# Kernel optimization log

Measured on AMD Instinct MI355X. Metric: run time of the kernel, lower is better.

Reference implementation:

```python
import jax, jax.numpy as jnp
import numpy as np

EPS = 1e-6

def _l2norm_axis1(x):
    # torch Normalize(2): divide by L2 norm over dim 1 (the T axis of [B,T,F])
    return x / jnp.sqrt(jnp.sum(x * x, axis=1, keepdims=True))

def _mlp(x, w1, b1, w2, b2):
    # frame_MLPEmbed / freq_MLPEmbed share structure: linear-relu-linear-l2norm(dim=1)
    h = jax.nn.relu(x @ w1 + b1)
    return _l2norm_axis1(h @ w2 + b2)

def _reshape_feat(f):
    # [L,B,C,T,D] -> permute(0,2,1,3) per layer -> [L,B,T,C*D]
    L, B, C, T, D = f.shape
    return jnp.transpose(f, (0, 1, 3, 2, 4)).reshape(L, B, T, C * D)

def _cos_time(x):
    # x: [L,B,T,C]; cosine sims between frames within each batch item -> [L,B,T,T]
    xn = x / (jnp.sqrt(jnp.sum(x * x, axis=-1, keepdims=True)) + EPS)
    S = (jnp.einsum('lbtc,lbsc->lbts', xn, xn) + 1.0) * 0.5
    return S / jnp.sum(S, axis=-1, keepdims=True)

def _cos_freq(x):
    # cosine sims between batch items per frame, returned as [L,B,T,B]
    xn = x / (jnp.sqrt(jnp.sum(x * x, axis=-1, keepdims=True)) + EPS)
    S = (jnp.einsum('lbtc,latc->lbta', xn, xn) + 1.0) * 0.5
    return S / jnp.sum(S, axis=-1, keepdims=True)

def _forward(feat_s, feat_t, tk_w1, tk_b1, tk_w2, tk_b2, fk_w1, fk_b1, fk_w2, fk_b2,
             tq_w1, tq_b1, tq_w2, tq_b2, fq_w1, fq_b1, fq_w2, fq_b2):
    feat_t = jax.lax.stop_gradient(feat_t)  # detach=True
    xs = _reshape_feat(feat_s)  # [s_len,B,T,CD]
    xt = _reshape_feat(feat_t)  # [t_len,B,T,CD]
    s_len, t_len = xs.shape[0], xt.shape[0]

    # gram matrices used for key/query MLPs
    sim_t = jnp.einsum('lbtc,lbsc->lbts', xt, xt)    # [t_len,B,T,T]
    sim_t_g = jnp.einsum('lbtc,latc->lbta', xt, xt)  # [t_len,B,T,B]
    sim_s = jnp.einsum('lbtc,lbsc->lbts', xs, xs)    # [s_len,B,T,T]
    sim_s_g = jnp.einsum('lbtc,latc->lbta', xs, xs)  # [s_len,B,T,B]

    mlp_v = jax.vmap(_mlp)  # vmap over the per-layer MLPs
    tk = mlp_v(sim_t, tk_w1, tk_b1, tk_w2, tk_b2)     # [t_len,B,T,T]
    fk = mlp_v(sim_t_g, fk_w1, fk_b1, fk_w2, fk_b2)   # [t_len,B,T,32]
    tq = mlp_v(sim_s, tq_w1, tq_b1, tq_w2, tq_b2)     # [s_len,B,T,T]
    fq = mlp_v(sim_s_g, fq_w1, fq_b1, fq_w2, fq_b2)   # [s_len,B,T,32]

    time_key = jnp.moveaxis(tk, 0, -1)    # [B,T,T,t_len]
    freq_key = jnp.moveaxis(fk, 0, -1)    # [B,T,32,t_len]
    time_query = jnp.moveaxis(tq, 0, 2)   # [B,T,s_len,T]
    freq_query = jnp.moveaxis(fq, 0, 2)   # [B,T,s_len,32]

    time_att = jax.nn.softmax(jnp.matmul(time_query, time_key), axis=-1)  # [B,T,s_len,t_len]
    freq_att = jax.nn.softmax(jnp.matmul(freq_query, freq_key), axis=-1)  # [B,T,s_len,t_len]

    stu_time = _cos_time(xs)  # [s_len,B,T,T]
    tea_time = _cos_time(xt)  # [t_len,B,T,T]
    stu_freq = _cos_freq(xs)  # [s_len,B,T,B]
    tea_freq = _cos_freq(xt)  # [t_len,B,T,B]

    # the torch nested lists are [i][j]; student entries depend only on i, teacher only on j
    stu_time_b = jnp.broadcast_to(stu_time[:, None], (s_len, t_len) + stu_time.shape[1:])
    stu_freq_b = jnp.broadcast_to(stu_freq[:, None], (s_len, t_len) + stu_freq.shape[1:])
    tea_time_b = jnp.broadcast_to(tea_time[None, :], (s_len, t_len) + tea_time.shape[1:])
    tea_freq_b = jnp.broadcast_to(tea_freq[None, :], (s_len, t_len) + tea_freq.shape[1:])

    return (stu_time_b, stu_freq_b, tea_time_b, tea_freq_b, time_att, freq_att)

def setup_inputs() -> dict:
    key = jax.random.key(0)
    ks = jax.random.split(key, 20)
    s_len, t_len, B, C, T, D = 4, 4, 8, 64, 256, 16
    H = 2 * T  # frame MLP hidden
    F = 32     # bsz * factor
    p = lambda k, shp: jax.random.normal(k, shp, dtype=jnp.float32) * 0.02
    return {
        'feat_s': jax.random.normal(ks[0], (s_len, B, C, T, D), dtype=jnp.float32),
        'feat_t': jax.random.normal(ks[1], (t_len, B, C, T, D), dtype=jnp.float32),
        'tk_w1': p(ks[2], (t_len, T, H)), 'tk_b1': p(ks[3], (t_len, H)),
        'tk_w2': p(ks[4], (t_len, H, T)), 'tk_b2': p(ks[5], (t_len, T)),
        'fk_w1': p(ks[6], (t_len, B, F)), 'fk_b1': p(ks[7], (t_len, F)),
        'fk_w2': p(ks[8], (t_len, F, F)), 'fk_b2': p(ks[9], (t_len, F)),
        'tq_w1': p(ks[10], (s_len, T, H)), 'tq_b1': p(ks[11], (s_len, H)),
        'tq_w2': p(ks[12], (s_len, H, T)), 'tq_b2': p(ks[13], (s_len, T)),
        'fq_w1': p(ks[14], (s_len, B, F)), 'fq_b1': p(ks[15], (s_len, F)),
        'fq_w2': p(ks[16], (s_len, F, F)), 'fq_b2': p(ks[17], (s_len, F)),
    }

def reference(feat_s, feat_t, tk_w1, tk_b1, tk_w2, tk_b2, fk_w1, fk_b1, fk_w2, fk_b2,
              tq_w1, tq_b1, tq_w2, tq_b2, fq_w1, fq_b1, fq_w2, fq_b2):
    return _forward(feat_s, feat_t, tk_w1, tk_b1, tk_w2, tk_b2, fk_w1, fk_b1, fk_w2, fk_b2,
                    tq_w1, tq_b1, tq_w2, tq_b2, fq_w1, fq_b1, fq_w2, fq_b2)
```

## Files before the change

### kernel.cpp

```cpp
#include <hip/hip_runtime.h>
#include <math.h>

typedef _Float16 half_t;
typedef _Float16 h2 __attribute__((ext_vector_type(2)));
typedef _Float16 h4 __attribute__((ext_vector_type(4)));
typedef _Float16 h8 __attribute__((ext_vector_type(8)));
typedef float f4 __attribute__((ext_vector_type(4)));
static constexpr float REPS = 1e-6f;

__global__ __launch_bounds__(256) void k_prep2(const float* __restrict__ tkw1, const float* __restrict__ tqw1,
                                               const float* __restrict__ tkw2, const float* __restrict__ tqw2,
                                               const float* __restrict__ tkb1, const float* __restrict__ tqb1,
                                               const float* __restrict__ tkb2, const float* __restrict__ tqb2,
                                               half_t* __restrict__ W1t, half_t* __restrict__ W2t,
                                               float* __restrict__ Bc1, float* __restrict__ Bc2,
                                               float* __restrict__ part,
                                               const float* __restrict__ fs, const float* __restrict__ ft,
                                               half_t* __restrict__ Xh, float* __restrict__ nrm) {
  __shared__ float T[64][65];
  int bid = blockIdx.x;
  int tid = threadIdx.x;
  if (bid < 256) {
    int z = bid >> 5, tile = bid & 31;
    int kt = tile >> 3, ntile = tile & 7;
    const float* src = (z < 4 ? tkw1 : tqw1) + (size_t)(z & 3) * 256 * 512;
#pragma unroll
    for (int q = 0; q < 16; q++) {
      int e = q * 256 + tid;
      int r = e >> 6, c = e & 63;
      T[r][c] = src[(size_t)(kt * 64 + r) * 512 + ntile * 64 + c];
    }
    __syncthreads();
#pragma unroll
    for (int q = 0; q < 16; q++) {
      int e = q * 256 + tid;
      int nn = e >> 6, kk = e & 63;
      W1t[(size_t)z * 512 * 256 + (size_t)(ntile * 64 + nn) * 256 + kt * 64 + kk] = (half_t)T[kk][nn];
    }
  } else if (bid < 512) {
    int bb = bid - 256;
    int z = bb >> 5, tile = bb & 31;
    int kt = tile >> 2, ntile = tile & 3;
    const float* src = (z < 4 ? tkw2 : tqw2) + (size_t)(z & 3) * 512 * 256;
#pragma unroll
    for (int q = 0; q < 16; q++) {
      int e = q * 256 + tid;
      int r = e >> 6, c = e & 63;
      T[r][c] = src[(size_t)(kt * 64 + r) * 256 + ntile * 64 + c];
    }
    __syncthreads();
#pragma unroll
    for (int q = 0; q < 16; q++) {
      int e = q * 256 + tid;
      int nn = e >> 6, kk = e & 63;
      W2t[(size_t)z * 256 * 512 + (size_t)(ntile * 64 + nn) * 512 + kt * 64 + kk] = (half_t)T[kk][nn];
    }
  } else if (bid == 512) {
    for (int e = tid; e < 4096; e += 256) {
      int z = e >> 9, n = e & 511;
      Bc1[e] = (z < 4 ? tkb1 : tqb1)[(z & 3) * 512 + n];
    }
    for (int e = tid; e < 2048; e += 256) {
      int z = e >> 8, n = e & 255;
      Bc2[e] = (z < 4 ? tkb2 : tqb2)[(z & 3) * 256 + n];
    }
    for (int e = tid; e < 16384; e += 256) part[e] = 0.f;
  } else {
    int bid2 = bid - 513;
    int tensor = bid2 >> 7;
    int l = (bid2 >> 5) & 3;
    int b = (bid2 >> 2) & 7;
    int tc = bid2 & 3;
    int tl = tid >> 2;
    int d0 = (tid & 3) * 4;
    int t = tc * 64 + tl;
    const float* base = (tensor ? ft : fs) + (size_t)((l * 8 + b) * 64) * 4096 + t * 16 + d0;
    size_t row = (size_t)(tensor * 32 + l * 8 + b) * 256 + t;
    half_t* xrow = Xh + row * 1024 + d0;
    float acc = 0.f;
#pragma unroll 8
    for (int c = 0; c < 64; c++) {
      float4 v = *(const float4*)(base + (size_t)c * 4096);
      acc += v.x * v.x + v.y * v.y + v.z * v.z + v.w * v.w;
      h4 hv;
      hv[0] = (half_t)v.x; hv[1] = (half_t)v.y; hv[2] = (half_t)v.z; hv[3] = (half_t)v.w;
      *(h4*)(xrow + c * 16) = hv;
    }
    acc += __shfl_xor(acc, 1);
    acc += __shfl_xor(acc, 2);
    if ((tid & 3) == 0) nrm[row] = sqrtf(acc);
  }
}

__global__ __launch_bounds__(512) void k_gs(const half_t* __restrict__ Xh,
                                            const float* __restrict__ nrm,
                                            half_t* __restrict__ simh,
                                            float* __restrict__ out_stu,
                                            float* __restrict__ out_tea,
                                            float* __restrict__ simg) {
  __shared__ __align__(16) char smem[35584];
  int bid = blockIdx.x;
  int tid = threadIdx.x;
  if (bid < 256) {
    half_t* Bsm = (half_t*)smem;
    float* Tile = (float*)smem;
    float* rspart = (float*)(smem + 33280);
    float* rowsumS = (float*)(smem + 34304);
    float* invn = (float*)(smem + 34560);
    int mt = bid & 3;
    int z = bid >> 2;
    const half_t* Bb = Xh + (size_t)z * 256 * 1024;
    int w = tid >> 6, lane = tid & 63;
    int wm = w >> 2, wn = w & 3;
    int lr = lane & 15, lg = lane >> 4;
    f4 acc[2][4] = {};
    int r0 = tid >> 3, seg0 = tid & 7;
    int sw0 = (seg0 ^ (r0 & 7)) * 8;
    h8 bv[4], bv2[4];
#pragma unroll
    for (int it = 0; it < 4; it++)
      bv[it] = *(const h8*)(Bb + (size_t)(it * 64 + r0) * 1024 + seg0 * 8);
    for (int kc = 0; kc < 1024; kc += 64) {
      __syncthreads();
#pragma unroll
      for (int it = 0; it < 4; it++)
        *(h8*)(Bsm + (it * 64 + r0) * 64 + sw0) = bv[it];
      __syncthreads();
      if (kc + 64 < 1024) {
#pragma unroll
        for (int it = 0; it < 4; it++)
          bv2[it] = *(const h8*)(Bb + (size_t)(it * 64 + r0) * 1024 + kc + 64 + seg0 * 8);
      }
#pragma unroll
      for (int kk = 0; kk < 2; kk++) {
        int g = kk * 4 + lg;
        h8 af[2], bf[4];
#pragma unroll
        for (int mf = 0; mf < 2; mf++) {
          int rA = mt * 64 + wm * 32 + mf * 16 + lr;
          af[mf] = *(const h8*)(Bsm + rA * 64 + ((g ^ (rA & 7)) * 8));
        }
#pragma unroll
        for (int nf = 0; nf < 4; nf++) {
          int rB = wn * 64 + nf * 16 + lr;
          bf[nf] = *(const h8*)(Bsm + rB * 64 + ((g ^ (rB & 7)) * 8));
        }
#pragma unroll
        for (int mf = 0; mf < 2; mf++)
#pragma unroll
          for (int nf = 0; nf < 4; nf++)
            acc[mf][nf] = __builtin_amdgcn_mfma_f32_16x16x32_f16(af[mf], bf[nf], acc[mf][nf], 0, 0, 0);
      }
      if (kc + 64 < 1024) {
#pragma unroll
        for (int it = 0; it < 4; it++) bv[it] = bv2[it];
      }
    }
    int tensor = z >> 5, l = (z >> 3) & 3, b = z & 7;
    const float* nz = nrm + z * 256;
    if (tid < 256) invn[tid] = 1.f / (nz[tid] + REPS);
    __syncthreads();
    int cols[4];
#pragma unroll
    for (int nf = 0; nf < 4; nf++) cols[nf] = wn * 64 + nf * 16 + lr;
    float rowpart[2][4];
#pragma unroll
    for (int mf = 0; mf < 2; mf++)
#pragma unroll
      for (int rg = 0; rg < 4; rg++) {
        int rib = wm * 32 + mf * 16 + lg * 4 + rg;
        float invr = invn[mt * 64 + rib];
        float p = 0.f;
#pragma unroll
        for (int nf = 0; nf < 4; nf++)
          p += fmaf(acc[mf][nf][rg] * (invr * invn[cols[nf]]), 0.5f, 0.5f);
        rowpart[mf][rg] = p;
      }
#pragma unroll
    for (int mf = 0; mf < 2; mf++)
#pragma unroll
      for (int rg = 0; rg < 4; rg++) {
        float p = rowpart[mf][rg];
        p += __shfl_xor(p, 1); p += __shfl_xor(p, 2);
        p += __shfl_xor(p, 4); p += __shfl_xor(p, 8);
        rowpart[mf][rg] = p;
      }
    if (lr == 0) {
#pragma unroll
      for (int mf = 0; mf < 2; mf++)
#pragma unroll
        for (int rg = 0; rg < 4; rg++)
          rspart[(wm * 32 + mf * 16 + lg * 4 + rg) * 4 + wn] = rowpart[mf][rg];
    }
    __syncthreads();
    if (tid < 64)
      rowsumS[tid] = 1.f / (rspart[tid * 4] + rspart[tid * 4 + 1] +
                            rspart[tid * 4 + 2] + rspart[tid * 4 + 3]);
    __syncthreads();
    float* outp = tensor ? out_tea : out_stu;
    for (int ph = 0; ph < 2; ph++) {
      if (wm == ph) {
#pragma unroll
        for (int mf = 0; mf < 2; mf++)
#pragma unroll
          for (int nf = 0; nf < 4; nf++)
#pragma unroll
            for (int rg = 0; rg < 4; rg++)
              Tile[(mf * 16 + lg * 4 + rg) * 260 + cols[nf]] = acc[mf][nf][rg];
      }
      __syncthreads();
#pragma unroll
      for (int it2 = 0; it2 < 4; it2++) {
        int fid = it2 * 512 + tid;
        int row = fid >> 6;
        int col = (fid & 63) << 2;
        int rib = ph * 32 + row;
        int t = mt * 64 + rib;
        float4 S4 = *(const float4*)(Tile + row * 260 + col);
        float invnr = invn[t];
        float rinv = rowsumS[rib];
        float4 vv;
        vv.x = fmaf(S4.x * (invnr * invn[col + 0]), 0.5f, 0.5f) * rinv;
        vv.y = fmaf(S4.y * (invnr * invn[col + 1]), 0.5f, 0.5f) * rinv;
        vv.z = fmaf(S4.z * (invnr * invn[col + 2]), 0.5f, 0.5f) * rinv;
        vv.w = fmaf(S4.w * (invnr * invn[col + 3]), 0.5f, 0.5f) * rinv;
        h4 sh;
        sh[0] = (half_t)S4.x; sh[1] = (half_t)S4.y;
        sh[2] = (half_t)S4.z; sh[3] = (half_t)S4.w;
        *(h4*)(simh + (size_t)z * 65536 + (size_t)t * 256 + col) = sh;
        size_t inner = ((size_t)(b * 256 + t)) * 256 + col;
        if (tensor == 0) {
          size_t base = (size_t)l * 4 * 524288;
#pragma unroll
          for (int j = 0; j < 4; j++)
            *(float4*)(outp + base + (size_t)j * 524288 + inner) = vv;
        } else {
#pragma unroll
          for (int i2 = 0; i2 < 4; i2++)
            *(float4*)(outp + ((size_t)(i2 * 4 + l)) * 524288 + inner) = vv;
        }
      }
      __syncthreads();
    }
  } else {
    half_t* X = (half_t*)smem;
    float* red = (float*)(smem + 33280);
    int sb = bid - 256;
    int tensor = sb >> 8;
    int l = (sb >> 6) & 3;
    int tc = sb & 63;
    int t0 = tc * 4;
    int kg = tid >> 8;
    int inner = tid & 255;
    int tl_c = inner >> 6;
    int ab = inner & 63;
    int bb = ab >> 3, aa = ab & 7;
    float acc = 0.f;
    for (int kh = 0; kh < 2; kh++) {
#pragma unroll
      for (int j = 0; j < 4; j++) {
        int i = j * 512 + tid;
        int r = i >> 6, col = i & 63;
        int b = r & 7, tl = r >> 3;
        const half_t* src = Xh + ((size_t)(tensor * 32 + l * 8 + b) * 256 + t0 + tl) * 1024
                               + kh * 512 + col * 8;
        *(h8*)(X + r * 520 + col * 8) = *(const h8*)src;
      }
      __syncthreads();
      {
        const half_t* xa = X + (tl_c * 8 + bb) * 520 + kg * 256;
        const half_t* xb = X + (tl_c * 8 + aa) * 520 + kg * 256;
#pragma unroll 8
        for (int k = 0; k < 256; k += 8) {
          h8 va = *(const h8*)(xa + k);
          h8 vb = *(const h8*)(xb + k);
#if __has_builtin(__builtin_amdgcn_fdot2)
#pragma unroll
          for (int i = 0; i < 4; i++) {
            h2 pa, pb;
            pa[0] = va[2 * i]; pa[1] = va[2 * i + 1];
            pb[0] = vb[2 * i]; pb[1] = vb[2 * i + 1];
            acc = __builtin_amdgcn_fdot2(pa, pb, acc, false);
          }
#else
#pragma unroll
          for (int e = 0; e < 8; e++) acc += (float)va[e] * (float)vb[e];
#endif
        }
      }
      __syncthreads();
    }
    if (kg == 1) red[inner] = acc;
    __syncthreads();
    if (kg == 0)
      simg[(size_t)tensor * 65536 + ((size_t)(l * 8 + bb) * 256 + t0 + tl_c) * 8 + aa] =
          acc + red[inner];
  }
}

__global__ __launch_bounds__(256) void k_m1s(const half_t* __restrict__ simh,
                                             const half_t* __restrict__ W1t,
                                             const float* __restrict__ Bc1,
                                             half_t* __restrict__ hbuf,
                                             const float* __restrict__ simg,
                                             const float* __restrict__ n,
                                             float* __restrict__ out_stu, float* __restrict__ out_tea,
                                             const float* __restrict__ qw1, const float* __restrict__ qb1,
                                             const float* __restrict__ qw2, const float* __restrict__ qb2,
                                             const float* __restrict__ kw1, const float* __restrict__ kb1,
                                             const float* __restrict__ kw2, const float* __restrict__ kb2,
                                             float* __restrict__ qout, float* __restrict__ kout) {
  __shared__ __align__(16) char smem[40352];
  int bid = blockIdx.x;
  int tid = threadIdx.x;
  if (bid < 512) {
    constexpr int K = 256, N = 512;
    half_t* Asm = (half_t*)smem;
    half_t* Bsm = (half_t*)(smem + 16384);
    int mt = bid & 15, nt = (bid >> 4) & 3, z = bid >> 6;
    int l = z & 3, path = z >> 2;
    const half_t* Ab = simh + ((size_t)((path == 0 ? 32 : 0) + l * 8)) * 256 * 256;
    const half_t* Bb = W1t + (size_t)z * 512 * 256;
    half_t* Ob = hbuf + (size_t)z * 2048 * 512;
    int wave = tid >> 6, lane = tid & 63;
    int wm = (wave >> 1) * 64, wn = (wave & 1) * 64;
    int lr = lane & 15, lg = lane >> 4;
    f4 acc[4][4] = {};
    int r0 = tid >> 3, seg0 = tid & 7;
    int sw0 = (seg0 ^ (r0 & 7)) * 8;
    h8 av[4], bv[4], av2[4], bv2[4];
#pragma unroll
    for (int j = 0; j < 4; j++) {
      av[j] = *(const h8*)(Ab + (size_t)(mt * 128 + r0 + 32 * j) * K + seg0 * 8);
      bv[j] = *(const h8*)(Bb + (size_t)(nt * 128 + r0 + 32 * j) * K + seg0 * 8);
    }
    for (int kc = 0; kc < K; kc += 64) {
      __syncthreads();
#pragma unroll
      for (int j = 0; j < 4; j++) {
        *(h8*)(Asm + (r0 + 32 * j) * 64 + sw0) = av[j];
        *(h8*)(Bsm + (r0 + 32 * j) * 64 + sw0) = bv[j];
      }
      __syncthreads();
      if (kc + 64 < K) {
#pragma unroll
        for (int j = 0; j < 4; j++) {
          av2[j] = *(const h8*)(Ab + (size_t)(mt * 128 + r0 + 32 * j) * K + kc + 64 + seg0 * 8);
          bv2[j] = *(const h8*)(Bb + (size_t)(nt * 128 + r0 + 32 * j) * K + kc + 64 + seg0 * 8);
        }
      }
#pragma unroll
      for (int kk = 0; kk < 2; kk++) {
        h8 af[4], bf[4];
#pragma unroll
        for (int mf = 0; mf < 4; mf++) {
          int r = wm + mf * 16 + lr;
          af[mf] = *(const h8*)(Asm + r * 64 + (((kk * 4 + lg) ^ (r & 7)) * 8));
        }
#pragma unroll
        for (int nf = 0; nf < 4; nf++) {
          int r = wn + nf * 16 + lr;
          bf[nf] = *(const h8*)(Bsm + r * 64 + (((kk * 4 + lg) ^ (r & 7)) * 8));
        }
#pragma unroll
        for (int mf = 0; mf < 4; mf++)
#pragma unroll
          for (int nf = 0; nf < 4; nf++)
            acc[mf][nf] = __builtin_amdgcn_mfma_f32_16x16x32_f16(af[mf], bf[nf], acc[mf][nf], 0, 0, 0);
      }
      if (kc + 64 < K) {
#pragma unroll
        for (int j = 0; j < 4; j++) { av[j] = av2[j]; bv[j] = bv2[j]; }
      }
    }
#pragma unroll
    for (int nf = 0; nf < 4; nf++) {
      int col = nt * 128 + wn + nf * 16 + lr;
      float bv3 = Bc1[z * N + col];
#pragma unroll
      for (int mf = 0; mf < 4; mf++) {
#pragma unroll
        for (int rg = 0; rg < 4; rg++) {
          int row = mt * 128 + wm + mf * 16 + lg * 4 + rg;
          float v = fmaxf(acc[mf][nf][rg] + bv3, 0.f);
          Ob[(size_t)row * N + col] = (half_t)v;
        }
      }
    }
  } else if (bid < 576) {
    int bb = bid - 512;
    int tensor = bb >> 5;
    int lb = bb & 31;
    const float* sg = simg + (size_t)tensor * 65536;
    const float* nb2 = n + tensor * 8192;
    float* out = tensor ? out_tea : out_stu;
    int l = lb >> 3, b = lb & 7;
    int a = tid & 7;
    for (int tc = 0; tc < 8; tc++) {
      int t = tc * 32 + (tid >> 3);
      float nb = nb2[lb * 256 + t] + REPS;
      float na = nb2[(l * 8 + a) * 256 + t] + REPS;
      float v = (sg[((size_t)lb * 256 + t) * 8 + a] / (nb * na) + 1.f) * 0.5f;
      float w = v;
      for (int m = 1; m < 8; m <<= 1) w += __shfl_xor(w, m);
      v /= w;
      size_t inner = ((size_t)(b * 256 + t)) * 8 + a;
      if (tensor == 0) {
#pragma unroll
        for (int j = 0; j < 4; j++) out[((size_t)(l * 4 + j)) * 16384 + inner] = v;
      } else {
#pragma unroll
        for (int i = 0; i < 4; i++) out[((size_t)(i * 4 + l)) * 16384 + inner] = v;
      }
    }
  } else {
    float* sw1 = (float*)smem;
    float* sb1 = (float*)(smem + 1024);
    float* sw2 = (float*)(smem + 1152);
    float* sb2 = (float*)(smem + 5248);
    float* zs  = (float*)(smem + 5376);
    float* pcn = (float*)(smem + 39168);
    float* cn  = (float*)(smem + 40224);
    int bb = bid - 576;
    int tensor = bb >> 5;
    int lb = bb & 31;
    int l = lb >> 3;
    const float* w1 = tensor ? kw1 : qw1;
    const float* b1 = tensor ? kb1 : qb1;
    const float* w2 = tensor ? kw2 : qw2;
    const float* b2 = tensor ? kb2 : qb2;
    const float* sg = simg + (size_t)tensor * 65536;
    float* outp = tensor ? kout : qout;
    int t = tid;
    sw1[t] = w1[l * 256 + t];
    if (t < 32) { sb1[t] = b1[l * 32 + t]; sb2[t] = b2[l * 32 + t]; }
    for (int q = t; q < 1024; q += 256) sw2[q] = w2[l * 1024 + q];
    __syncthreads();
    float x[8];
#pragma unroll
    for (int a = 0; a < 8; a++) x[a] = sg[((size_t)lb * 256 + t) * 8 + a];
    float h[32];
#pragma unroll
    for (int f = 0; f < 32; f++) {
      float acc = sb1[f];
#pragma unroll
      for (int a = 0; a < 8; a++) acc += x[a] * sw1[a * 32 + f];
      h[f] = fmaxf(acc, 0.f);
    }
#pragma unroll
    for (int g = 0; g < 32; g++) {
      float acc = sb2[g];
#pragma unroll
      for (int f = 0; f < 32; f++) acc += h[f] * sw2[f * 32 + g];
      zs[t * 33 + g] = acc;
    }
    __syncthreads();
    {
      int col = t & 31, ch = t >> 5;
      float sq = 0.f;
      for (int r = ch * 32; r < ch * 32 + 32; r++) { float v = zs[r * 33 + col]; sq += v * v; }
      pcn[ch * 33 + col] = sq;
    }
    __syncthreads();
    if (t < 32) {
      float ssum = 0.f;
#pragma unroll
      for (int c = 0; c < 8; c++) ssum += pcn[c * 33 + t];
      cn[t] = sqrtf(ssum);
    }
    __syncthreads();
#pragma unroll
    for (int g = 0; g < 32; g++)
      outp[((size_t)lb * 256 + t) * 32 + g] = zs[t * 33 + g] / cn[g];
  }
}

__global__ __launch_bounds__(256) void k_mfma2(const half_t* __restrict__ A,
                                               const half_t* __restrict__ Bt,
                                               const float* __restrict__ bias,
                                               half_t* __restrict__ out,
                                               float* __restrict__ part) {
  constexpr int K = 512, N = 256;
  __shared__ __align__(16) half_t Asm[128 * 64];
  __shared__ __align__(16) half_t Bsm[128 * 64];
  int z = blockIdx.z;
  const half_t* Ab = A + (size_t)z * 2048 * 512;
  const half_t* Bb = Bt + (size_t)z * 256 * 512;
  half_t* Ob = out + (size_t)z * 2048 * 256;
  int mt = blockIdx.x, nt = blockIdx.y;
  int tid = threadIdx.x;
  int wave = tid >> 6, lane = tid & 63;
  int wm = (wave >> 1) * 64, wn = (wave & 1) * 64;
  int lr = lane & 15, lg = lane >> 4;
  f4 acc[4][4] = {};
  int r0 = tid >> 3, seg0 = tid & 7;
  int sw0 = (seg0 ^ (r0 & 7)) * 8;
  h8 av[4], bv[4], av2[4], bv2[4];
#pragma unroll
  for (int j = 0; j < 4; j++) {
    av[j] = *(const h8*)(Ab + (size_t)(mt * 128 + r0 + 32 * j) * K + seg0 * 8);
    bv[j] = *(const h8*)(Bb + (size_t)(nt * 128 + r0 + 32 * j) * K + seg0 * 8);
  }
  for (int kc = 0; kc < K; kc += 64) {
    __syncthreads();
#pragma unroll
    for (int j = 0; j < 4; j++) {
      *(h8*)(Asm + (r0 + 32 * j) * 64 + sw0) = av[j];
      *(h8*)(Bsm + (r0 + 32 * j) * 64 + sw0) = bv[j];
    }
    __syncthreads();
    if (kc + 64 < K) {
#pragma unroll
      for (int j = 0; j < 4; j++) {
        av2[j] = *(const h8*)(Ab + (size_t)(mt * 128 + r0 + 32 * j) * K + kc + 64 + seg0 * 8);
        bv2[j] = *(const h8*)(Bb + (size_t)(nt * 128 + r0 + 32 * j) * K + kc + 64 + seg0 * 8);
      }
    }
#pragma unroll
    for (int kk = 0; kk < 2; kk++) {
      h8 af[4], bf[4];
#pragma unroll
      for (int mf = 0; mf < 4; mf++) {
        int r = wm + mf * 16 + lr;
        af[mf] = *(const h8*)(Asm + r * 64 + (((kk * 4 + lg) ^ (r & 7)) * 8));
      }
#pragma unroll
      for (int nf = 0; nf < 4; nf++) {
        int r = wn + nf * 16 + lr;
        bf[nf] = *(const h8*)(Bsm + r * 64 + (((kk * 4 + lg) ^ (r & 7)) * 8));
      }
#pragma unroll
      for (int mf = 0; mf < 4; mf++)
#pragma unroll
        for (int nf = 0; nf < 4; nf++)
          acc[mf][nf] = __builtin_amdgcn_mfma_f32_16x16x32_f16(af[mf], bf[nf], acc[mf][nf], 0, 0, 0);
    }
    if (kc + 64 < K) {
#pragma unroll
      for (int j = 0; j < 4; j++) { av[j] = av2[j]; bv[j] = bv2[j]; }
    }
  }
#pragma unroll
  for (int nf = 0; nf < 4; nf++) {
    int col = nt * 128 + wn + nf * 16 + lr;
    float bv3 = bias[z * N + col];
    float colsq = 0.f;
#pragma unroll
    for (int mf = 0; mf < 4; mf++) {
#pragma unroll
      for (int rg = 0; rg < 4; rg++) {
        int row = mt * 128 + wm + mf * 16 + lg * 4 + rg;
        float v = acc[mf][nf][rg] + bv3;
        Ob[(size_t)row * N + col] = (half_t)v;
        colsq += v * v;
      }
    }
    colsq += __shfl_xor(colsq, 16);
    colsq += __shfl_xor(colsq, 32);
    if (lg == 0) {
      int b = mt >> 1;
      atomicAdd(&part[((z * 8 + b) << 8) + col], colsq);
    }
  }
}

__global__ __launch_bounds__(256) void k_att(const half_t* __restrict__ Zq,
                                             const half_t* __restrict__ Zk,
                                             const float* __restrict__ part,
                                             const float* __restrict__ fq,
                                             const float* __restrict__ fk,
                                             float* __restrict__ out_time,
                                             float* __restrict__ out_freq) {
  __shared__ float invq[4][256], invk[4][256];
  int bid = blockIdx.x;
  int tid = threadIdx.x;
  if (bid < 128) {
    int b = bid >> 4, tc = bid & 15;
    for (int e = tid; e < 1024; e += 256) {
      int i = e >> 8, s = e & 255;
      invq[i][s] = rsqrtf(part[(((4 + i) * 8 + b) << 8) + s]);
      invk[i][s] = rsqrtf(part[((i * 8 + b) << 8) + s]);
    }
    __syncthreads();
    int w = tid >> 6, lane = tid & 63;
    int s0 = lane * 4;
#pragma unroll
    for (int tt = 0; tt < 4; tt++) {
      int t = tc * 16 + w * 4 + tt;
      float qv[4][4], kv[4][4];
#pragma unroll
      for (int i = 0; i < 4; i++) {
        size_t lbO = (size_t)(i * 8 + b);
        h4 qh = *(const h4*)(Zq + (lbO * 256 + t) * 256 + s0);
        h4 kh = *(const h4*)(Zk + (lbO * 256 + t) * 256 + s0);
#pragma unroll
        for (int e = 0; e < 4; e++) {
          qv[i][e] = (float)qh[e] * invq[i][s0 + e];
          kv[i][e] = (float)kh[e] * invk[i][s0 + e];
        }
      }
      float acc[4][4];
#pragma unroll
      for (int i = 0; i < 4; i++)
#pragma unroll
        for (int j = 0; j < 4; j++) {
          float a = 0.f;
#pragma unroll
          for (int e = 0; e < 4; e++) a += qv[i][e] * kv[j][e];
          acc[i][j] = a;
        }
#pragma unroll
      for (int i = 0; i < 4; i++)
#pragma unroll
        for (int j = 0; j < 4; j++)
          for (int m = 32; m >= 1; m >>= 1) acc[i][j] += __shfl_xor(acc[i][j], m);
      if (lane < 16) {
        int i = lane >> 2, j = lane & 3;
        float mx = fmaxf(fmaxf(acc[i][0], acc[i][1]), fmaxf(acc[i][2], acc[i][3]));
        float sum = expf(acc[i][0] - mx) + expf(acc[i][1] - mx) + expf(acc[i][2] - mx) + expf(acc[i][3] - mx);
        out_time[((size_t)(b * 256 + t)) * 16 + lane] = expf(acc[i][j] - mx) / sum;
      }
    }
  } else {
    int sub = tid >> 6, lane = tid & 63;
    int pair = (bid - 128) * 4 + sub;
    int b = pair >> 7, tp = pair & 127;
    int t = tp * 2 + (lane >> 5);
    int f = lane & 31;
    float qv[4], kv[4];
#pragma unroll
    for (int i = 0; i < 4; i++) {
      size_t lbO = (size_t)(i * 8 + b);
      qv[i] = fq[(lbO * 256 + t) * 32 + f];
      kv[i] = fk[(lbO * 256 + t) * 32 + f];
    }
    float acc[4][4];
#pragma unroll
    for (int i = 0; i < 4; i++)
#pragma unroll
      for (int j = 0; j < 4; j++) acc[i][j] = qv[i] * kv[j];
#pragma unroll
    for (int i = 0; i < 4; i++)
#pragma unroll
      for (int j = 0; j < 4; j++)
        for (int m = 16; m >= 1; m >>= 1) acc[i][j] += __shfl_xor(acc[i][j], m);
    int fl = lane & 31;
    if (fl < 16) {
      int i = fl >> 2, j = fl & 3;
      float mx = fmaxf(fmaxf(acc[i][0], acc[i][1]), fmaxf(acc[i][2], acc[i][3]));
      float sum = expf(acc[i][0] - mx) + expf(acc[i][1] - mx) + expf(acc[i][2] - mx) + expf(acc[i][3] - mx);
      out_freq[((size_t)(b * 256 + t)) * 16 + fl] = expf(acc[i][j] - mx) / sum;
    }
  }
}

extern "C" void kernel_launch(void* const* d_in, const int* in_sizes, int n_in,
                              void* d_out, int out_size, void* d_ws, size_t ws_size,
                              hipStream_t stream) {
  (void)in_sizes; (void)n_in; (void)out_size; (void)ws_size;
  const float* feat_s = (const float*)d_in[0];
  const float* feat_t = (const float*)d_in[1];
  const float* tk_w1 = (const float*)d_in[2];
  const float* tk_b1 = (const float*)d_in[3];
  const float* tk_w2 = (const float*)d_in[4];
  const float* tk_b2 = (const float*)d_in[5];
  const float* fk_w1 = (const float*)d_in[6];
  const float* fk_b1 = (const float*)d_in[7];
  const float* fk_w2 = (const float*)d_in[8];
  const float* fk_b2 = (const float*)d_in[9];
  const float* tq_w1 = (const float*)d_in[10];
  const float* tq_b1 = (const float*)d_in[11];
  const float* tq_w2 = (const float*)d_in[12];
  const float* tq_b2 = (const float*)d_in[13];
  const float* fq_w1 = (const float*)d_in[14];
  const float* fq_b1 = (const float*)d_in[15];
  const float* fq_w2 = (const float*)d_in[16];
  const float* fq_b2 = (const float*)d_in[17];

  float* ws = (float*)d_ws;
  half_t* Xh   = (half_t*)ws;
  half_t* hbuf = (half_t*)ws;
  half_t* Zbuf = (half_t*)(ws + 4194304);
  half_t* simh = (half_t*)(ws + 8388608);
  half_t* W1t  = (half_t*)(ws + 10485760);
  half_t* W2t  = (half_t*)(ws + 11010048);
  float* Bc1   = ws + 11534336;
  float* Bc2   = ws + 11538432;
  float* simg  = ws + 11540480;
  float* nrm   = ws + 11671552;
  float* part  = ws + 11687936;
  float* fkb   = ws + 11704320;
  float* fqb   = ws + 11966464;

  float* out = (float*)d_out;
  float* out_stu_time = out;
  float* out_stu_freq = out + 8388608;
  float* out_tea_time = out + 8650752;
  float* out_tea_freq = out + 17039360;
  float* out_time_att = out + 17301504;
  float* out_freq_att = out + 17334272;

  hipLaunchKernelGGL(k_prep2, dim3(769), dim3(256), 0, stream,
                     tk_w1, tq_w1, tk_w2, tq_w2, tk_b1, tq_b1, tk_b2, tq_b2,
                     W1t, W2t, Bc1, Bc2, part, feat_s, feat_t, Xh, nrm);
  hipLaunchKernelGGL(k_gs, dim3(768), dim3(512), 0, stream,
                     Xh, nrm, simh, out_stu_time, out_tea_time, simg);
  hipLaunchKernelGGL(k_m1s, dim3(640), dim3(256), 0, stream,
                     simh, W1t, Bc1, hbuf, simg, nrm,
                     out_stu_freq, out_tea_freq,
                     fq_w1, fq_b1, fq_w2, fq_b2, fk_w1, fk_b1, fk_w2, fk_b2, fqb, fkb);
  hipLaunchKernelGGL(k_mfma2, dim3(16, 2, 8), dim3(256), 0, stream,
                     hbuf, W2t, Bc2, Zbuf, part);
  hipLaunchKernelGGL(k_att, dim3(384), dim3(256), 0, stream,
                     Zbuf + (size_t)4 * 2048 * 256, Zbuf, part, fqb, fkb,
                     out_time_att, out_freq_att);
}
```

Baseline: 105.0 us.

## Rebalance kernel stages: move weight prep into gram kernel, freq attention into GEMM

Weight transpose/convert and bias/part init move from the first kernel into extra blocks of the gram-similarity kernel. The first kernel now only converts features, with 8 elements per thread. Frequency attention blocks move into the second GEMM kernel so they run alongside it, and the time-attention kernel shrinks to its own grid. The aim is to shorten the critical path and fill idle CUs during the GEMM, at the cost of larger heterogeneous grids. The gram kernel's per-phase __syncthreads is also made conditional (ph==0), which could be a correctness risk.

```diff
diff --git a/kernel.cpp b/kernel.cpp
--- a/kernel.cpp
+++ b/kernel.cpp
@@ -8,88 +8,36 @@
 typedef float f4 __attribute__((ext_vector_type(4)));
 static constexpr float REPS = 1e-6f;
 
-__global__ __launch_bounds__(256) void k_prep2(const float* __restrict__ tkw1, const float* __restrict__ tqw1,
-                                               const float* __restrict__ tkw2, const float* __restrict__ tqw2,
-                                               const float* __restrict__ tkb1, const float* __restrict__ tqb1,
-                                               const float* __restrict__ tkb2, const float* __restrict__ tqb2,
-                                               half_t* __restrict__ W1t, half_t* __restrict__ W2t,
-                                               float* __restrict__ Bc1, float* __restrict__ Bc2,
-                                               float* __restrict__ part,
-                                               const float* __restrict__ fs, const float* __restrict__ ft,
-                                               half_t* __restrict__ Xh, float* __restrict__ nrm) {
-  __shared__ float T[64][65];
+__global__ __launch_bounds__(256) void k_x2h(const float* __restrict__ fs,
+                                             const float* __restrict__ ft,
+                                             half_t* __restrict__ Xh,
+                                             float* __restrict__ nrm) {
   int bid = blockIdx.x;
+  int tensor = bid >> 6;
+  int l = (bid >> 4) & 3;
+  int b = (bid >> 1) & 7;
+  int th = bid & 1;
   int tid = threadIdx.x;
-  if (bid < 256) {
-    int z = bid >> 5, tile = bid & 31;
-    int kt = tile >> 3, ntile = tile & 7;
-    const float* src = (z < 4 ? tkw1 : tqw1) + (size_t)(z & 3) * 256 * 512;
-#pragma unroll
-    for (int q = 0; q < 16; q++) {
-      int e = q * 256 + tid;
-      int r = e >> 6, c = e & 63;
-      T[r][c] = src[(size_t)(kt * 64 + r) * 512 + ntile * 64 + c];
-    }
-    __syncthreads();
-#pragma unroll
-    for (int q = 0; q < 16; q++) {
-      int e = q * 256 + tid;
-      int nn = e >> 6, kk = e & 63;
-      W1t[(size_t)z * 512 * 256 + (size_t)(ntile * 64 + nn) * 256 + kt * 64 + kk] = (half_t)T[kk][nn];
-    }
-  } else if (bid < 512) {
-    int bb = bid - 256;
-    int z = bb >> 5, tile = bb & 31;
-    int kt = tile >> 2, ntile = tile & 3;
-    const float* src = (z < 4 ? tkw2 : tqw2) + (size_t)(z & 3) * 512 * 256;
-#pragma unroll
-    for (int q = 0; q < 16; q++) {
-      int e = q * 256 + tid;
-      int r = e >> 6, c = e & 63;
-      T[r][c] = src[(size_t)(kt * 64 + r) * 256 + ntile * 64 + c];
-    }
-    __syncthreads();
-#pragma unroll
-    for (int q = 0; q < 16; q++) {
-      int e = q * 256 + tid;
-      int nn = e >> 6, kk = e & 63;
-      W2t[(size_t)z * 256 * 512 + (size_t)(ntile * 64 + nn) * 512 + kt * 64 + kk] = (half_t)T[kk][nn];
-    }
-  } else if (bid == 512) {
-    for (int e = tid; e < 4096; e += 256) {
-      int z = e >> 9, n = e & 511;
-      Bc1[e] = (z < 4 ? tkb1 : tqb1)[(z & 3) * 512 + n];
-    }
-    for (int e = tid; e < 2048; e += 256) {
-      int z = e >> 8, n = e & 255;
-      Bc2[e] = (z < 4 ? tkb2 : tqb2)[(z & 3) * 256 + n];
-    }
-    for (int e = tid; e < 16384; e += 256) part[e] = 0.f;
-  } else {
-    int bid2 = bid - 513;
-    int tensor = bid2 >> 7;
-    int l = (bid2 >> 5) & 3;
-    int b = (bid2 >> 2) & 7;
-    int tc = bid2 & 3;
-    int tl = tid >> 2;
-    int d0 = (tid & 3) * 4;
-    int t = tc * 64 + tl;
-    const float* base = (tensor ? ft : fs) + (size_t)((l * 8 + b) * 64) * 4096 + t * 16 + d0;
-    size_t row = (size_t)(tensor * 32 + l * 8 + b) * 256 + t;
-    half_t* xrow = Xh + row * 1024 + d0;
-    float acc = 0.f;
+  int tl = tid >> 1;
+  int d0 = (tid & 1) * 8;
+  int t = th * 128 + tl;
+  const float* base = (tensor ? ft : fs) + (size_t)((l * 8 + b) * 64) * 4096 + t * 16 + d0;
+  size_t row = (size_t)(tensor * 32 + l * 8 + b) * 256 + t;
+  half_t* xrow = Xh + row * 1024 + d0;
+  float acc = 0.f;
 #pragma unroll 8
-    for (int c = 0; c < 64; c++) {
-      float4 v = *(const float4*)(base + (size_t)c * 4096);
-      acc += v.x * v.x + v.y * v.y + v.z * v.z + v.w * v.w;
-      h4 hv;
-      hv[0] = (half_t)v.x; hv[1] = (half_t)v.y; hv[2] = (half_t)v.z; hv[3] = (half_t)v.w;
-      *(h4*)(xrow + c * 16) = hv;
-    }
-    acc += __shfl_xor(acc, 1);
-    acc += __shfl_xor(acc, 2);
-    if ((tid & 3) == 0) nrm[row] = sqrtf(acc);
+  for (int c = 0; c < 64; c++) {
+    float4 v1 = *(const float4*)(base + (size_t)c * 4096);
+    float4 v2 = *(const float4*)(base + (size_t)c * 4096 + 4);
+    acc += v1.x * v1.x + v1.y * v1.y + v1.z * v1.z + v1.w * v1.w;
+    acc += v2.x * v2.x + v2.y * v2.y + v2.z * v2.z + v2.w * v2.w;
+    h8 hv;
+    hv[0] = (half_t)v1.x; hv[1] = (half_t)v1.y; hv[2] = (half_t)v1.z; hv[3] = (half_t)v1.w;
+    hv[4] = (half_t)v2.x; hv[5] = (half_t)v2.y; hv[6] = (half_t)v2.z; hv[7] = (half_t)v2.w;
+    *(h8*)(xrow + c * 16) = hv;
   }
+  acc += __shfl_xor(acc, 1);
+  if ((tid & 1) == 0) nrm[row] = sqrtf(acc);
 }
 
 __global__ __launch_bounds__(512) void k_gs(const half_t* __restrict__ Xh,
@@ -97,7 +45,14 @@
                                             half_t* __restrict__ simh,
                                             float* __restrict__ out_stu,
                                             float* __restrict__ out_tea,
-                                            float* __restrict__ simg) {
+                                            float* __restrict__ simg,
+                                            const float* __restrict__ tkw1, const float* __restrict__ tqw1,
+                                            const float* __restrict__ tkw2, const float* __restrict__ tqw2,
+                                            const float* __restrict__ tkb1, const float* __restrict__ tqb1,
+                                            const float* __restrict__ tkb2, const float* __restrict__ tqb2,
+                                            half_t* __restrict__ W1t, half_t* __restrict__ W2t,
+                                            float* __restrict__ Bc1, float* __restrict__ Bc2,
+                                            float* __restrict__ part) {
   __shared__ __align__(16) char smem[35584];
   int bid = blockIdx.x;
   int tid = threadIdx.x;
@@ -240,9 +195,9 @@
             *(float4*)(outp + ((size_t)(i2 * 4 + l)) * 524288 + inner) = vv;
         }
       }
-      __syncthreads();
-    }
-  } else {
+      if (ph == 0) __syncthreads();
+    }
+  } else if (bid < 768) {
     half_t* X = (half_t*)smem;
     float* red = (float*)(smem + 33280);
     int sb = bid - 256;
@@ -295,6 +250,55 @@
     if (kg == 0)
       simg[(size_t)tensor * 65536 + ((size_t)(l * 8 + bb) * 256 + t0 + tl_c) * 8 + aa] =
           acc + red[inner];
+  } else if (bid < 1280) {
+    float (*T)[65] = (float(*)[65])smem;
+    int wb = bid - 768;
+    if (wb < 256) {
+      int z = wb >> 5, tile = wb & 31;
+      int kt = tile >> 3, ntile = tile & 7;
+      const float* src = (z < 4 ? tkw1 : tqw1) + (size_t)(z & 3) * 256 * 512;
+#pragma unroll
+      for (int q = 0; q < 8; q++) {
+        int e = q * 512 + tid;
+        int r = e >> 6, c = e & 63;
+        T[r][c] = src[(size_t)(kt * 64 + r) * 512 + ntile * 64 + c];
+      }
+      __syncthreads();
+#pragma unroll
+      for (int q = 0; q < 8; q++) {
+        int e = q * 512 + tid;
+        int nn = e >> 6, kk = e & 63;
+        W1t[(size_t)z * 512 * 256 + (size_t)(ntile * 64 + nn) * 256 + kt * 64 + kk] = (half_t)T[kk][nn];
+      }
+    } else {
+      int bb2 = wb - 256;
+      int z = bb2 >> 5, tile = bb2 & 31;
+      int kt = tile >> 2, ntile = tile & 3;
+      const float* src = (z < 4 ? tkw2 : tqw2) + (size_t)(z & 3) * 512 * 256;
+#pragma unroll
+      for (int q = 0; q < 8; q++) {
+        int e = q * 512 + tid;
+        int r = e >> 6, c = e & 63;
+        T[r][c] = src[(size_t)(kt * 64 + r) * 256 + ntile * 64 + c];
+      }
+      __syncthreads();
+#pragma unroll
+      for (int q = 0; q < 8; q++) {
+        int e = q * 512 + tid;
+        int nn = e >> 6, kk = e & 63;
+        W2t[(size_t)z * 256 * 512 + (size_t)(ntile * 64 + nn) * 512 + kt * 64 + kk] = (half_t)T[kk][nn];
+      }
+    }
+  } else {
+    for (int e = tid; e < 4096; e += 512) {
+      int z = e >> 9, n = e & 511;
+      Bc1[e] = (z < 4 ? tkb1 : tqb1)[(z & 3) * 512 + n];
+    }
+    for (int e = tid; e < 2048; e += 512) {
+      int z = e >> 8, n = e & 255;
+      Bc2[e] = (z < 4 ? tkb2 : tqb2)[(z & 3) * 256 + n];
+    }
+    for (int e = tid; e < 16384; e += 512) part[e] = 0.f;
   }
 }
 
@@ -475,155 +479,101 @@
   }
 }
 
-__global__ __launch_bounds__(256) void k_mfma2(const half_t* __restrict__ A,
-                                               const half_t* __restrict__ Bt,
-                                               const float* __restrict__ bias,
-                                               half_t* __restrict__ out,
-                                               float* __restrict__ part) {
-  constexpr int K = 512, N = 256;
-  __shared__ __align__(16) half_t Asm[128 * 64];
-  __shared__ __align__(16) half_t Bsm[128 * 64];
-  int z = blockIdx.z;
-  const half_t* Ab = A + (size_t)z * 2048 * 512;
-  const half_t* Bb = Bt + (size_t)z * 256 * 512;
-  half_t* Ob = out + (size_t)z * 2048 * 256;
-  int mt = blockIdx.x, nt = blockIdx.y;
-  int tid = threadIdx.x;
-  int wave = tid >> 6, lane = tid & 63;
-  int wm = (wave >> 1) * 64, wn = (wave & 1) * 64;
-  int lr = lane & 15, lg = lane >> 4;
-  f4 acc[4][4] = {};
-  int r0 = tid >> 3, seg0 = tid & 7;
-  int sw0 = (seg0 ^ (r0 & 7)) * 8;
-  h8 av[4], bv[4], av2[4], bv2[4];
-#pragma unroll
-  for (int j = 0; j < 4; j++) {
-    av[j] = *(const h8*)(Ab + (size_t)(mt * 128 + r0 + 32 * j) * K + seg0 * 8);
-    bv[j] = *(const h8*)(Bb + (size_t)(nt * 128 + r0 + 32 * j) * K + seg0 * 8);
-  }
-  for (int kc = 0; kc < K; kc += 64) {
-    __syncthreads();
-#pragma unroll
-    for (int j = 0; j < 4; j++) {
-      *(h8*)(Asm + (r0 + 32 * j) * 64 + sw0) = av[j];
-      *(h8*)(Bsm + (r0 + 32 * j) * 64 + sw0) = bv[j];
-    }
-    __syncthreads();
-    if (kc + 64 < K) {
-#pragma unroll
-      for (int j = 0; j < 4; j++) {
-        av2[j] = *(const h8*)(Ab + (size_t)(mt * 128 + r0 + 32 * j) * K + kc + 64 + seg0 * 8);
-        bv2[j] = *(const h8*)(Bb + (size_t)(nt * 128 + r0 + 32 * j) * K + kc + 64 + seg0 * 8);
-      }
-    }
-#pragma unroll
-    for (int kk = 0; kk < 2; kk++) {
-      h8 af[4], bf[4];
-#pragma unroll
-      for (int mf = 0; mf < 4; mf++) {
-        int r = wm + mf * 16 + lr;
-        af[mf] = *(const h8*)(Asm + r * 64 + (((kk * 4 + lg) ^ (r & 7)) * 8));
-      }
-#pragma unroll
-      for (int nf = 0; nf < 4; nf++) {
-        int r = wn + nf * 16 + lr;
-        bf[nf] = *(const h8*)(Bsm + r * 64 + (((kk * 4 + lg) ^ (r & 7)) * 8));
-      }
-#pragma unroll
-      for (int mf = 0; mf < 4; mf++)
-#pragma unroll
-        for (int nf = 0; nf < 4; nf++)
-          acc[mf][nf] = __builtin_amdgcn_mfma_f32_16x16x32_f16(af[mf], bf[nf], acc[mf][nf], 0, 0, 0);
-    }
-    if (kc + 64 < K) {
-#pragma unroll
-      for (int j = 0; j < 4; j++) { av[j] = av2[j]; bv[j] = bv2[j]; }
-    }
-  }
-#pragma unroll
-  for (int nf = 0; nf < 4; nf++) {
-    int col = nt * 128 + wn + nf * 16 + lr;
-    float bv3 = bias[z * N + col];
-    float colsq = 0.f;
-#pragma unroll
-    for (int mf = 0; mf < 4; mf++) {
-#pragma unroll
-      for (int rg = 0; rg < 4; rg++) {
-        int row = mt * 128 + wm + mf * 16 + lg * 4 + rg;
-        float v = acc[mf][nf][rg] + bv3;
-        Ob[(size_t)row * N + col] = (half_t)v;
-        colsq += v * v;
-      }
-    }
-    colsq += __shfl_xor(colsq, 16);
-    colsq += __shfl_xor(colsq, 32);
-    if (lg == 0) {
-      int b = mt >> 1;
-      atomicAdd(&part[((z * 8 + b) << 8) + col], colsq);
-    }
-  }
-}
-
-__global__ __launch_bounds__(256) void k_att(const half_t* __restrict__ Zq,
-                                             const half_t* __restrict__ Zk,
-                                             const float* __restrict__ part,
+__global__ __launch_bounds__(256) void k_m2a(const half_t* __restrict__ A,
+                                             const half_t* __restrict__ Bt,
+                                             const float* __restrict__ bias,
+                                             half_t* __restrict__ out,
+                                             float* __restrict__ part,
                                              const float* __restrict__ fq,
                                              const float* __restrict__ fk,
-                                             float* __restrict__ out_time,
                                              float* __restrict__ out_freq) {
-  __shared__ float invq[4][256], invk[4][256];
+  __shared__ __align__(16) char smem[32768];
   int bid = blockIdx.x;
   int tid = threadIdx.x;
-  if (bid < 128) {
-    int b = bid >> 4, tc = bid & 15;
-    for (int e = tid; e < 1024; e += 256) {
-      int i = e >> 8, s = e & 255;
-      invq[i][s] = rsqrtf(part[(((4 + i) * 8 + b) << 8) + s]);
-      invk[i][s] = rsqrtf(part[((i * 8 + b) << 8) + s]);
-    }
-    __syncthreads();
-    int w = tid >> 6, lane = tid & 63;
-    int s0 = lane * 4;
-#pragma unroll
-    for (int tt = 0; tt < 4; tt++) {
-      int t = tc * 16 + w * 4 + tt;
-      float qv[4][4], kv[4][4];
-#pragma unroll
-      for (int i = 0; i < 4; i++) {
-        size_t lbO = (size_t)(i * 8 + b);
-        h4 qh = *(const h4*)(Zq + (lbO * 256 + t) * 256 + s0);
-        h4 kh = *(const h4*)(Zk + (lbO * 256 + t) * 256 + s0);
-#pragma unroll
-        for (int e = 0; e < 4; e++) {
-          qv[i][e] = (float)qh[e] * invq[i][s0 + e];
-          kv[i][e] = (float)kh[e] * invk[i][s0 + e];
-        }
-      }
-      float acc[4][4];
-#pragma unroll
-      for (int i = 0; i < 4; i++)
+  if (bid < 256) {
+    constexpr int K = 512, N = 256;
+    half_t* Asm = (half_t*)smem;
+    half_t* Bsm = (half_t*)(smem + 16384);
+    int mt = bid & 15, nt = (bid >> 4) & 1, z = bid >> 5;
+    const half_t* Ab = A + (size_t)z * 2048 * 512;
+    const half_t* Bb = Bt + (size_t)z * 256 * 512;
+    half_t* Ob = out + (size_t)z * 2048 * 256;
+    int wave = tid >> 6, lane = tid & 63;
+    int wm = (wave >> 1) * 64, wn = (wave & 1) * 64;
+    int lr = lane & 15, lg = lane >> 4;
+    f4 acc[4][4] = {};
+    int r0 = tid >> 3, seg0 = tid & 7;
+    int sw0 = (seg0 ^ (r0 & 7)) * 8;
+    h8 av[4], bv[4], av2[4], bv2[4];
+#pragma unroll
+    for (int j = 0; j < 4; j++) {
+      av[j] = *(const h8*)(Ab + (size_t)(mt * 128 + r0 + 32 * j) * K + seg0 * 8);
+      bv[j] = *(const h8*)(Bb + (size_t)(nt * 128 + r0 + 32 * j) * K + seg0 * 8);
+    }
+    for (int kc = 0; kc < K; kc += 64) {
+      __syncthreads();
+#pragma unroll
+      for (int j = 0; j < 4; j++) {
+        *(h8*)(Asm + (r0 + 32 * j) * 64 + sw0) = av[j];
+        *(h8*)(Bsm + (r0 + 32 * j) * 64 + sw0) = bv[j];
+      }
+      __syncthreads();
+      if (kc + 64 < K) {
 #pragma unroll
         for (int j = 0; j < 4; j++) {
-          float a = 0.f;
-#pragma unroll
-          for (int e = 0; e < 4; e++) a += qv[i][e] * kv[j][e];
-          acc[i][j] = a;
-        }
-#pragma unroll
-      for (int i = 0; i < 4; i++)
-#pragma unroll
-        for (int j = 0; j < 4; j++)
-          for (int m = 32; m >= 1; m >>= 1) acc[i][j] += __shfl_xor(acc[i][j], m);
-      if (lane < 16) {
-        int i = lane >> 2, j = lane & 3;
-        float mx = fmaxf(fmaxf(acc[i][0], acc[i][1]), fmaxf(acc[i][2], acc[i][3]));
-        float sum = expf(acc[i][0] - mx) + expf(acc[i][1] - mx) + expf(acc[i][2] - mx) + expf(acc[i][3] - mx);
-        out_time[((size_t)(b * 256 + t)) * 16 + lane] = expf(acc[i][j] - mx) / sum;
+          av2[j] = *(const h8*)(Ab + (size_t)(mt * 128 + r0 + 32 * j) * K + kc + 64 + seg0 * 8);
+          bv2[j] = *(const h8*)(Bb + (size_t)(nt * 128 + r0 + 32 * j) * K + kc + 64 + seg0 * 8);
+        }
+      }
+#pragma unroll
+      for (int kk = 0; kk < 2; kk++) {
+        h8 af[4], bf[4];
+#pragma unroll
+        for (int mf = 0; mf < 4; mf++) {
+          int r = wm + mf * 16 + lr;
+          af[mf] = *(const h8*)(Asm + r * 64 + (((kk * 4 + lg) ^ (r & 7)) * 8));
+        }
+#pragma unroll
+        for (int nf = 0; nf < 4; nf++) {
+          int r = wn + nf * 16 + lr;
+          bf[nf] = *(const h8*)(Bsm + r * 64 + (((kk * 4 + lg) ^ (r & 7)) * 8));
+        }
+#pragma unroll
+        for (int mf = 0; mf < 4; mf++)
+#pragma unroll
+          for (int nf = 0; nf < 4; nf++)
+            acc[mf][nf] = __builtin_amdgcn_mfma_f32_16x16x32_f16(af[mf], bf[nf], acc[mf][nf], 0, 0, 0);
+      }
+      if (kc + 64 < K) {
+#pragma unroll
+        for (int j = 0; j < 4; j++) { av[j] = av2[j]; bv[j] = bv2[j]; }
+      }
+    }
+#pragma unroll
+    for (int nf = 0; nf < 4; nf++) {
+      int col = nt * 128 + wn + nf * 16 + lr;
+      float bv3 = bias[z * N + col];
+      float colsq = 0.f;
+#pragma unroll
+      for (int mf = 0; mf < 4; mf++) {
+#pragma unroll
+        for (int rg = 0; rg < 4; rg++) {
+          int row = mt * 128 + wm + mf * 16 + lg * 4 + rg;
+          float v = acc[mf][nf][rg] + bv3;
+          Ob[(size_t)row * N + col] = (half_t)v;
+          colsq += v * v;
+        }
+      }
+      colsq += __shfl_xor(colsq, 16);
+      colsq += __shfl_xor(colsq, 32);
+      if (lg == 0) {
+        int b = mt >> 1;
+        atomicAdd(&part[((z * 8 + b) << 8) + col], colsq);
       }
     }
   } else {
     int sub = tid >> 6, lane = tid & 63;
-    int pair = (bid - 128) * 4 + sub;
+    int pair = (bid - 256) * 4 + sub;
     int b = pair >> 7, tp = pair & 127;
     int t = tp * 2 + (lane >> 5);
     int f = lane & 31;
@@ -650,6 +600,61 @@
       float mx = fmaxf(fmaxf(acc[i][0], acc[i][1]), fmaxf(acc[i][2], acc[i][3]));
       float sum = expf(acc[i][0] - mx) + expf(acc[i][1] - mx) + expf(acc[i][2] - mx) + expf(acc[i][3] - mx);
       out_freq[((size_t)(b * 256 + t)) * 16 + fl] = expf(acc[i][j] - mx) / sum;
+    }
+  }
+}
+
+__global__ __launch_bounds__(256) void k_att(const half_t* __restrict__ Zq,
+                                             const half_t* __restrict__ Zk,
+                                             const float* __restrict__ part,
+                                             float* __restrict__ out_time) {
+  __shared__ float invq[4][256], invk[4][256];
+  int bid = blockIdx.x;
+  int tid = threadIdx.x;
+  int b = bid >> 4, tc = bid & 15;
+  for (int e = tid; e < 1024; e += 256) {
+    int i = e >> 8, s = e & 255;
+    invq[i][s] = rsqrtf(part[(((4 + i) * 8 + b) << 8) + s]);
+    invk[i][s] = rsqrtf(part[((i * 8 + b) << 8) + s]);
+  }
+  __syncthreads();
+  int w = tid >> 6, lane = tid & 63;
+  int s0 = lane * 4;
+#pragma unroll
+  for (int tt = 0; tt < 4; tt++) {
+    int t = tc * 16 + w * 4 + tt;
+    float qv[4][4], kv[4][4];
+#pragma unroll
+    for (int i = 0; i < 4; i++) {
+      size_t lbO = (size_t)(i * 8 + b);
+      h4 qh = *(const h4*)(Zq + (lbO * 256 + t) * 256 + s0);
+      h4 kh = *(const h4*)(Zk + (lbO * 256 + t) * 256 + s0);
+#pragma unroll
+      for (int e = 0; e < 4; e++) {
+        qv[i][e] = (float)qh[e] * invq[i][s0 + e];
+        kv[i][e] = (float)kh[e] * invk[i][s0 + e];
+      }
+    }
+    float acc[4][4];
+#pragma unroll
+    for (int i = 0; i < 4; i++)
+#pragma unroll
+      for (int j = 0; j < 4; j++) {
+        float a = 0.f;
+#pragma unroll
+        for (int e = 0; e < 4; e++) a += qv[i][e] * kv[j][e];
+        acc[i][j] = a;
+      }
+#pragma unroll
+    for (int i = 0; i < 4; i++)
+#pragma unroll
+      for (int j = 0; j < 4; j++)
+        for (int m = 32; m >= 1; m >>= 1) acc[i][j] += __shfl_xor(acc[i][j], m);
+    if (lane < 16) {
+      int i = lane >> 2, j = lane & 3;
+      float mx = fmaxf(fmaxf(acc[i][0], acc[i][1]), fmaxf(acc[i][2], acc[i][3]));
+      float sum = expf(acc[i][0] - mx) + expf(acc[i][1] - mx) + expf(acc[i][2] - mx) + expf(acc[i][3] - mx);
+      out_time[((size_t)(b * 256 + t)) * 16 + lane] = expf(acc[i][j] - mx) / sum;
     }
   }
 }
@@ -700,18 +705,17 @@
   float* out_time_att = out + 17301504;
   float* out_freq_att = out + 17334272;
 
-  hipLaunchKernelGGL(k_prep2, dim3(769), dim3(256), 0, stream,
+  hipLaunchKernelGGL(k_x2h, dim3(128), dim3(256), 0, stream, feat_s, feat_t, Xh, nrm);
+  hipLaunchKernelGGL(k_gs, dim3(1281), dim3(512), 0, stream,
+                     Xh, nrm, simh, out_stu_time, out_tea_time, simg,
                      tk_w1, tq_w1, tk_w2, tq_w2, tk_b1, tq_b1, tk_b2, tq_b2,
-                     W1t, W2t, Bc1, Bc2, part, feat_s, feat_t, Xh, nrm);
-  hipLaunchKernelGGL(k_gs, dim3(768), dim3(512), 0, stream,
-                     Xh, nrm, simh, out_stu_time, out_tea_time, simg);
+                     W1t, W2t, Bc1, Bc2, part);
   hipLaunchKernelGGL(k_m1s, dim3(640), dim3(256), 0, stream,
                      simh, W1t, Bc1, hbuf, simg, nrm,
                      out_stu_freq, out_tea_freq,
                      fq_w1, fq_b1, fq_w2, fq_b2, fk_w1, fk_b1, fk_w2, fk_b2, fqb, fkb);
-  hipLaunchKernelGGL(k_mfma2, dim3(16, 2, 8), dim3(256), 0, stream,
-                     hbuf, W2t, Bc2, Zbuf, part);
-  hipLaunchKernelGGL(k_att, dim3(384), dim3(256), 0, stream,
-                     Zbuf + (size_t)4 * 2048 * 256, Zbuf, part, fqb, fkb,
-                     out_time_att, out_freq_att);
+  hipLaunchKernelGGL(k_m2a, dim3(512), dim3(256), 0, stream,
+                     hbuf, W2t, Bc2, Zbuf, part, fqb, fkb, out_freq_att);
+  hipLaunchKernelGGL(k_att, dim3(128), dim3(256), 0, stream,
+                     Zbuf + (size_t)4 * 2048 * 256, Zbuf, part, out_time_att);
 }
```

Measured after the change: 115.3 us. +9.8%, slower.

## Split feature conversion over channel quarters and store partial squared norms

Applied to the files above, without the earlier changes.

The feature-conversion part of the prep kernel now splits the 64-channel loop into four quarters, giving four times as many blocks. Each block writes a partial sum of squares instead of a final norm, and the consumer kernels add the four partials and take the square root. The aim is more memory-level parallelism in the bandwidth-bound fp32-to-fp16 conversion. It also drops one trailing barrier in the similarity epilogue, which risks a shared-memory hazard if that barrier was needed.

```diff
diff --git a/kernel.cpp b/kernel.cpp
--- a/kernel.cpp
+++ b/kernel.cpp
@@ -16,7 +16,7 @@
                                                float* __restrict__ Bc1, float* __restrict__ Bc2,
                                                float* __restrict__ part,
                                                const float* __restrict__ fs, const float* __restrict__ ft,
-                                               half_t* __restrict__ Xh, float* __restrict__ nrm) {
+                                               half_t* __restrict__ Xh, float* __restrict__ nsq) {
   __shared__ float T[64][65];
   int bid = blockIdx.x;
   int tid = threadIdx.x;
@@ -67,10 +67,11 @@
     for (int e = tid; e < 16384; e += 256) part[e] = 0.f;
   } else {
     int bid2 = bid - 513;
-    int tensor = bid2 >> 7;
-    int l = (bid2 >> 5) & 3;
-    int b = (bid2 >> 2) & 7;
-    int tc = bid2 & 3;
+    int tensor = bid2 >> 9;
+    int l = (bid2 >> 7) & 3;
+    int b = (bid2 >> 4) & 7;
+    int tc = (bid2 >> 2) & 3;
+    int cq = bid2 & 3;
     int tl = tid >> 2;
     int d0 = (tid & 3) * 4;
     int t = tc * 64 + tl;
@@ -78,8 +79,8 @@
     size_t row = (size_t)(tensor * 32 + l * 8 + b) * 256 + t;
     half_t* xrow = Xh + row * 1024 + d0;
     float acc = 0.f;
-#pragma unroll 8
-    for (int c = 0; c < 64; c++) {
+#pragma unroll
+    for (int c = cq * 16; c < cq * 16 + 16; c++) {
       float4 v = *(const float4*)(base + (size_t)c * 4096);
       acc += v.x * v.x + v.y * v.y + v.z * v.z + v.w * v.w;
       h4 hv;
@@ -88,12 +89,12 @@
     }
     acc += __shfl_xor(acc, 1);
     acc += __shfl_xor(acc, 2);
-    if ((tid & 3) == 0) nrm[row] = sqrtf(acc);
+    if ((tid & 3) == 0) nsq[cq * 16384 + row] = acc;
   }
 }
 
 __global__ __launch_bounds__(512) void k_gs(const half_t* __restrict__ Xh,
-                                            const float* __restrict__ nrm,
+                                            const float* __restrict__ nsq,
                                             half_t* __restrict__ simh,
                                             float* __restrict__ out_stu,
                                             float* __restrict__ out_tea,
@@ -157,8 +158,11 @@
       }
     }
     int tensor = z >> 5, l = (z >> 3) & 3, b = z & 7;
-    const float* nz = nrm + z * 256;
-    if (tid < 256) invn[tid] = 1.f / (nz[tid] + REPS);
+    if (tid < 256) {
+      int row = z * 256 + tid;
+      float s = nsq[row] + nsq[16384 + row] + nsq[32768 + row] + nsq[49152 + row];
+      invn[tid] = 1.f / (sqrtf(s) + REPS);
+    }
     __syncthreads();
     int cols[4];
 #pragma unroll
@@ -240,7 +244,7 @@
             *(float4*)(outp + ((size_t)(i2 * 4 + l)) * 524288 + inner) = vv;
         }
       }
-      __syncthreads();
+      if (ph == 0) __syncthreads();
     }
   } else {
     half_t* X = (half_t*)smem;
@@ -303,7 +307,7 @@
                                              const float* __restrict__ Bc1,
                                              half_t* __restrict__ hbuf,
                                              const float* __restrict__ simg,
-                                             const float* __restrict__ n,
+                                             const float* __restrict__ nsq,
                                              float* __restrict__ out_stu, float* __restrict__ out_tea,
                                              const float* __restrict__ qw1, const float* __restrict__ qb1,
                                              const float* __restrict__ qw2, const float* __restrict__ qb2,
@@ -388,18 +392,25 @@
       }
     }
   } else if (bid < 576) {
+    float* sn = (float*)smem;
     int bb = bid - 512;
     int tensor = bb >> 5;
     int lb = bb & 31;
     const float* sg = simg + (size_t)tensor * 65536;
-    const float* nb2 = n + tensor * 8192;
     float* out = tensor ? out_tea : out_stu;
     int l = lb >> 3, b = lb & 7;
+    for (int e = tid; e < 2048; e += 256) {
+      int a = e >> 8, t = e & 255;
+      int row = tensor * 8192 + (l * 8 + a) * 256 + t;
+      float s = nsq[row] + nsq[16384 + row] + nsq[32768 + row] + nsq[49152 + row];
+      sn[a * 256 + t] = sqrtf(s) + REPS;
+    }
+    __syncthreads();
     int a = tid & 7;
     for (int tc = 0; tc < 8; tc++) {
       int t = tc * 32 + (tid >> 3);
-      float nb = nb2[lb * 256 + t] + REPS;
-      float na = nb2[(l * 8 + a) * 256 + t] + REPS;
+      float nb = sn[b * 256 + t];
+      float na = sn[a * 256 + t];
       float v = (sg[((size_t)lb * 256 + t) * 8 + a] / (nb * na) + 1.f) * 0.5f;
       float w = v;
       for (int m = 1; m < 8; m <<= 1) w += __shfl_xor(w, m);
@@ -687,10 +698,10 @@
   float* Bc1   = ws + 11534336;
   float* Bc2   = ws + 11538432;
   float* simg  = ws + 11540480;
-  float* nrm   = ws + 11671552;
-  float* part  = ws + 11687936;
-  float* fkb   = ws + 11704320;
-  float* fqb   = ws + 11966464;
+  float* nsq   = ws + 11671552;
+  float* part  = ws + 11737088;
+  float* fkb   = ws + 11753472;
+  float* fqb   = ws + 12015616;
 
   float* out = (float*)d_out;
   float* out_stu_time = out;
@@ -700,13 +711,13 @@
   float* out_time_att = out + 17301504;
   float* out_freq_att = out + 17334272;
 
-  hipLaunchKernelGGL(k_prep2, dim3(769), dim3(256), 0, stream,
+  hipLaunchKernelGGL(k_prep2, dim3(1537), dim3(256), 0, stream,
                      tk_w1, tq_w1, tk_w2, tq_w2, tk_b1, tq_b1, tk_b2, tq_b2,
-                     W1t, W2t, Bc1, Bc2, part, feat_s, feat_t, Xh, nrm);
+                     W1t, W2t, Bc1, Bc2, part, feat_s, feat_t, Xh, nsq);
   hipLaunchKernelGGL(k_gs, dim3(768), dim3(512), 0, stream,
-                     Xh, nrm, simh, out_stu_time, out_tea_time, simg);
+                     Xh, nsq, simh, out_stu_time, out_tea_time, simg);
   hipLaunchKernelGGL(k_m1s, dim3(640), dim3(256), 0, stream,
-                     simh, W1t, Bc1, hbuf, simg, nrm,
+                     simh, W1t, Bc1, hbuf, simg, nsq,
                      out_stu_freq, out_tea_freq,
                      fq_w1, fq_b1, fq_w2, fq_b2, fk_w1, fk_b1, fk_w2, fk_b2, fqb, fkb);
   hipLaunchKernelGGL(k_mfma2, dim3(16, 2, 8), dim3(256), 0, stream,
```

After: 105.2 us. About the same (+0.2%).
